# Kernel tuning notes

Measured on AMD Instinct MI355X. Metric: run time of the kernel, lower is better.

Reference implementation:

```python
import jax, jax.numpy as jnp
import numpy as np

B, S, H, D, DM = 2, 512, 8, 32, 256  # batch, seq_len, n_head, d_k, d_model


def setup_inputs() -> dict:
    key = jax.random.key(0)
    ks = jax.random.split(key, 8)
    scale = 0.02
    return {
        "hidden_states": jax.random.normal(ks[0], (B, S, DM), dtype=jnp.float32),
        "rpe": jax.random.normal(ks[1], (B, S, S, D), dtype=jnp.float32),
        "w_q": jax.random.normal(ks[2], (DM, H * D), dtype=jnp.float32) * scale,
        "w_k": jax.random.normal(ks[3], (DM, H * D), dtype=jnp.float32) * scale,
        "w_v": jax.random.normal(ks[4], (DM, H * D), dtype=jnp.float32) * scale,
        "fc_w": jax.random.normal(ks[5], (H * D, DM), dtype=jnp.float32) * scale,
        "fc_b": jnp.zeros((DM,), dtype=jnp.float32),
        "ln_w": jnp.ones((DM,), dtype=jnp.float32),
        "ln_b": jnp.zeros((DM,), dtype=jnp.float32),
        "station_num": 256,
    }


def reference(hidden_states, rpe, w_q, w_k, w_v, fc_w, fc_b, ln_w, ln_b, station_num):
    b, s, dm = hidden_states.shape
    d = rpe.shape[-1]
    h = w_q.shape[1] // d

    def heads(x, w):
        # (b, s, dm) @ (dm, h*d) -> (b, h, s, d)
        return (x @ w).reshape(b, s, h, d).transpose(0, 2, 1, 3)

    q = heads(hidden_states, w_q)
    k = heads(hidden_states, w_k)
    v = heads(hidden_states, w_v)

    # torch: (q.unsqueeze(2) * k.unsqueeze(3) * rpe.unsqueeze(1)).sum(-1)
    # scores[b,h,i,j] = sum_d q[b,h,j,d] * k[b,h,i,d] * rpe[b,i,j,d]
    scores = jnp.einsum('bhjd,bhid,bijd->bhij', q, k, rpe) / jnp.sqrt(jnp.float32(d))

    # shielded mask: column j visible if j < station_num, plus the diagonal
    col = jnp.arange(s) < station_num                  # (s,)
    mask = col[None, :] | jnp.eye(s, dtype=bool)        # (s, s)
    scores = jnp.where(mask[None, None], scores, jnp.float32(-1e10))

    attn = jax.nn.softmax(scores, axis=-1)              # (b, h, s, s)
    out = jnp.einsum('bhij,bhjd->bhid', attn, v)        # (b, h, s, d)
    out = out.transpose(0, 2, 1, 3).reshape(b, s, h * d)

    ctx = out @ fc_w + fc_b + hidden_states             # residual
    mu = jnp.mean(ctx, axis=-1, keepdims=True)
    var = jnp.mean(jnp.square(ctx - mu), axis=-1, keepdims=True)
    ctx = (ctx - mu) / jnp.sqrt(var + 1e-6) * ln_w + ln_b
    return ctx
```

## Files before the change

kernel.cpp:

```cpp
#include <hip/hip_runtime.h>
#include <hip/hip_bf16.h>

#define B_  2
#define S_  512
#define H_  8
#define D_  32
#define DM_ 256
#define HD_ 256
#define NROW 4
#define TI  4

__global__ __launch_bounds__(256) void qkv_kernel(
    const float* __restrict__ hid, const float* __restrict__ wq,
    const float* __restrict__ wk, const float* __restrict__ wv,
    float* __restrict__ qo, float* __restrict__ ko, float* __restrict__ vo)
{
  __shared__ float hs[NROW][DM_];
  const int r0 = blockIdx.x * NROW;
  const float* w   = (blockIdx.y == 0) ? wq : (blockIdx.y == 1) ? wk : wv;
  float*       out = (blockIdx.y == 0) ? qo : (blockIdx.y == 1) ? ko : vo;
  const int tid = threadIdx.x;

  for (int idx = tid; idx < NROW * DM_; idx += 256)
    hs[idx >> 8][idx & 255] = hid[r0 * DM_ + idx];
  __syncthreads();

  float acc[NROW] = {0.f, 0.f, 0.f, 0.f};
  const float* wp = w + tid;
  #pragma unroll 8
  for (int c4 = 0; c4 < DM_ / 4; ++c4) {
    const float w0 = wp[(4 * c4 + 0) * HD_];
    const float w1 = wp[(4 * c4 + 1) * HD_];
    const float w2 = wp[(4 * c4 + 2) * HD_];
    const float w3 = wp[(4 * c4 + 3) * HD_];
    #pragma unroll
    for (int r = 0; r < NROW; ++r) {
      const float4 hv = reinterpret_cast<const float4*>(&hs[r][0])[c4];
      acc[r] = fmaf(hv.x, w0, acc[r]);
      acc[r] = fmaf(hv.y, w1, acc[r]);
      acc[r] = fmaf(hv.z, w2, acc[r]);
      acc[r] = fmaf(hv.w, w3, acc[r]);
    }
  }
  const int h = tid >> 5, d = tid & 31;
  #pragma unroll
  for (int r = 0; r < NROW; ++r) {
    const int g = r0 + r;
    const int b = g >> 9, s = g & (S_ - 1);
    out[((b * H_ + h) * S_ + s) * D_ + d] = acc[r];
  }
}

__device__ __forceinline__ float red8(float x) {
  int i;
  i = __builtin_amdgcn_mov_dpp(__float_as_int(x), 0xB1, 0xf, 0xf, true);
  x += __int_as_float(i);
  i = __builtin_amdgcn_mov_dpp(__float_as_int(x), 0x4E, 0xf, 0xf, true);
  x += __int_as_float(i);
  i = __builtin_amdgcn_mov_dpp(__float_as_int(x), 0x124, 0xf, 0xf, true);
  x += __int_as_float(i);
  return x;
}

__global__ __launch_bounds__(256, 8) void attn_kernel(
    const float* __restrict__ rpe, const float* __restrict__ q_ws,
    const float* __restrict__ k_ws, const float* __restrict__ v_ws,
    const int* __restrict__ station_p, float* __restrict__ o_ws)
{
  __shared__ float p_smem[TI * S_];
  __shared__ float sums[TI];

  const int tid  = threadIdx.x;
  const int w    = tid >> 6, lane = tid & 63;
  const int j8   = lane >> 3, dc = lane & 7;
  const int n    = blockIdx.x;
  const int h    = (n >> 3) & 7;
  const int t    = (n & 7) | ((n >> 6) << 3);
  const int b    = t >> 7;
  const int i0   = (t & 127) * TI;

  int station = station_p[0];
  station = station > S_ ? S_ : (station < 0 ? 0 : station);

  const float* qb = q_ws + (size_t)((b * H_ + h) * S_) * D_;
  const float* kb = k_ws + (size_t)((b * H_ + h) * S_ + i0) * D_;
  const float* vb = v_ws + (size_t)((b * H_ + h) * S_) * D_;
  const float* rb = rpe + ((size_t)b * S_ + i0) * S_ * D_;
  const float sc = 0.17677669529663687f;

  float4 kf[TI];
  #pragma unroll
  for (int ii = 0; ii < TI; ++ii)
    kf[ii] = *reinterpret_cast<const float4*>(kb + ii * D_ + dc * 4);

  for (int jb = w * 8; jb < station; jb += 32) {
    const int j  = jb + j8;
    const int jc = j < S_ ? j : S_ - 1;
    const float4 q4 = *reinterpret_cast<const float4*>(qb + jc * D_ + dc * 4);
    float4 rv[TI];
    #pragma unroll
    for (int ii = 0; ii < TI; ++ii)
      rv[ii] = *reinterpret_cast<const float4*>(
          rb + ii * (S_ * D_) + jc * D_ + dc * 4);
    #pragma unroll
    for (int ii = 0; ii < TI; ++ii) {
      float s = q4.x * kf[ii].x * rv[ii].x;
      s = fmaf(q4.y * kf[ii].y, rv[ii].y, s);
      s = fmaf(q4.z * kf[ii].z, rv[ii].z, s);
      s = fmaf(q4.w * kf[ii].w, rv[ii].w, s);
      s = red8(s);
      if (dc == 0 && j < station) p_smem[ii * S_ + j] = s * sc;
    }
  }
  if (w == 0 && j8 < TI) {
    const int j = i0 + j8;
    if (j >= station) {
      const float4 q4 = *reinterpret_cast<const float4*>(qb + j * D_ + dc * 4);
      const float4 rv = *reinterpret_cast<const float4*>(
          rb + j8 * (S_ * D_) + j * D_ + dc * 4);
      float s = q4.x * kf[j8].x * rv.x;
      s = fmaf(q4.y * kf[j8].y, rv.y, s);
      s = fmaf(q4.z * kf[j8].z, rv.z, s);
      s = fmaf(q4.w * kf[j8].w, rv.w, s);
      s = red8(s);
      if (dc == 0) p_smem[j8 * S_ + j] = s * sc;
    }
  }
  __syncthreads();

  {
    const int r  = w;
    const int ig = i0 + r;
    const bool dx = (ig >= station);
    float m = -1e30f;
    for (int jj = lane; jj < station; jj += 64) m = fmaxf(m, p_smem[r * S_ + jj]);
    const float dv = dx ? p_smem[r * S_ + ig] : -1e30f;
    m = fmaxf(m, dv);
    #pragma unroll
    for (int o = 32; o; o >>= 1) m = fmaxf(m, __shfl_xor(m, o, 64));
    float sum = 0.f;
    for (int jj = lane; jj < station; jj += 64) {
      const float e = __expf(p_smem[r * S_ + jj] - m);
      p_smem[r * S_ + jj] = e;
      sum += e;
    }
    #pragma unroll
    for (int o = 32; o; o >>= 1) sum += __shfl_xor(sum, o, 64);
    if (dx) {
      const float e = __expf(dv - m);
      sum += e;
      if (lane == 0) p_smem[r * S_ + ig] = e;
    }
    if (lane == 0) sums[r] = sum;
  }
  __syncthreads();

  float4 acc[TI];
  #pragma unroll
  for (int ii = 0; ii < TI; ++ii) acc[ii] = make_float4(0.f, 0.f, 0.f, 0.f);

  for (int jb = w * 8; jb < station; jb += 32) {
    const int j  = jb + j8;
    const int jc = j < S_ ? j : S_ - 1;
    const float4 v4 = *reinterpret_cast<const float4*>(vb + jc * D_ + dc * 4);
    #pragma unroll
    for (int ii = 0; ii < TI; ++ii) {
      float pv = 0.f;
      if (j < station) pv = p_smem[ii * S_ + j];
      acc[ii].x = fmaf(pv, v4.x, acc[ii].x);
      acc[ii].y = fmaf(pv, v4.y, acc[ii].y);
      acc[ii].z = fmaf(pv, v4.z, acc[ii].z);
      acc[ii].w = fmaf(pv, v4.w, acc[ii].w);
    }
  }
  if (w == 0 && j8 == 0) {
    #pragma unroll
    for (int ii = 0; ii < TI; ++ii) {
      const int ig = i0 + ii;
      if (ig >= station) {
        const float pv = p_smem[ii * S_ + ig];
        const float4 v4 = *reinterpret_cast<const float4*>(vb + ig * D_ + dc * 4);
        acc[ii].x = fmaf(pv, v4.x, acc[ii].x);
        acc[ii].y = fmaf(pv, v4.y, acc[ii].y);
        acc[ii].z = fmaf(pv, v4.z, acc[ii].z);
        acc[ii].w = fmaf(pv, v4.w, acc[ii].w);
      }
    }
  }
  __syncthreads();

  float4* redv = reinterpret_cast<float4*>(p_smem);
  #pragma unroll
  for (int ii = 0; ii < TI; ++ii) {
    float4 a = acc[ii];
    a.x += __shfl_xor(a.x, 8);
    a.y += __shfl_xor(a.y, 8);
    a.z += __shfl_xor(a.z, 8);
    a.w += __shfl_xor(a.w, 8);
    if ((j8 & 1) == 0)
      redv[((w * 4 + (j8 >> 1)) * TI + ii) * 8 + dc] = a;
  }
  __syncthreads();
  if (tid < TI * 8) {
    const int ii = tid >> 3, d4 = tid & 7;
    float4 a = make_float4(0.f, 0.f, 0.f, 0.f);
    #pragma unroll
    for (int g = 0; g < 16; ++g) {
      const float4 x = redv[(g * TI + ii) * 8 + d4];
      a.x += x.x; a.y += x.y; a.z += x.z; a.w += x.w;
    }
    const float inv = 1.f / sums[ii];
    a.x *= inv; a.y *= inv; a.z *= inv; a.w *= inv;
    reinterpret_cast<float4*>(
        o_ws + (size_t)((b * H_ + h) * S_ + i0 + ii) * D_)[d4] = a;
  }
}

__global__ __launch_bounds__(256) void fc_ln_kernel(
    const float* __restrict__ o_ws, const float* __restrict__ fc_w,
    const float* __restrict__ fc_b, const float* __restrict__ hid,
    const float* __restrict__ ln_w, const float* __restrict__ ln_b,
    float* __restrict__ out)
{
  __shared__ float orow[NROW][HD_];
  __shared__ float red[NROW][4];
  const int tid = threadIdx.x;
  const int r0 = blockIdx.x * NROW;

  for (int idx = tid; idx < NROW * HD_; idx += 256) {
    const int r = idx >> 8, m = idx & 255;
    const int g = r0 + r;
    const int b = g >> 9, i = g & (S_ - 1);
    orow[r][m] = o_ws[((b * H_ + (m >> 5)) * S_ + i) * D_ + (m & 31)];
  }
  __syncthreads();

  float acc[NROW] = {0.f, 0.f, 0.f, 0.f};
  const float* wp = fc_w + tid;
  #pragma unroll 8
  for (int n4 = 0; n4 < HD_ / 4; ++n4) {
    const float w0 = wp[(4 * n4 + 0) * DM_];
    const float w1 = wp[(4 * n4 + 1) * DM_];
    const float w2 = wp[(4 * n4 + 2) * DM_];
    const float w3 = wp[(4 * n4 + 3) * DM_];
    #pragma unroll
    for (int r = 0; r < NROW; ++r) {
      const float4 ov = reinterpret_cast<const float4*>(&orow[r][0])[n4];
      acc[r] = fmaf(ov.x, w0, acc[r]);
      acc[r] = fmaf(ov.y, w1, acc[r]);
      acc[r] = fmaf(ov.z, w2, acc[r]);
      acc[r] = fmaf(ov.w, w3, acc[r]);
    }
  }
  const float bias = fc_b[tid];
  #pragma unroll
  for (int r = 0; r < NROW; ++r) acc[r] += bias + hid[(r0 + r) * DM_ + tid];

  const int w = tid >> 6, lane = tid & 63;
  float mu[NROW];
  #pragma unroll
  for (int r = 0; r < NROW; ++r) {
    float s = acc[r];
    #pragma unroll
    for (int o = 32; o; o >>= 1) s += __shfl_xor(s, o, 64);
    if (lane == 0) red[r][w] = s;
  }
  __syncthreads();
  #pragma unroll
  for (int r = 0; r < NROW; ++r)
    mu[r] = (red[r][0] + red[r][1] + red[r][2] + red[r][3]) * (1.f / DM_);
  __syncthreads();
  #pragma unroll
  for (int r = 0; r < NROW; ++r) {
    const float dd = acc[r] - mu[r];
    float s = dd * dd;
    #pragma unroll
    for (int o = 32; o; o >>= 1) s += __shfl_xor(s, o, 64);
    if (lane == 0) red[r][w] = s;
  }
  __syncthreads();
  const float lw = ln_w[tid], lb = ln_b[tid];
  #pragma unroll
  for (int r = 0; r < NROW; ++r) {
    const float var = (red[r][0] + red[r][1] + red[r][2] + red[r][3]) * (1.f / DM_);
    out[(r0 + r) * DM_ + tid] =
        (acc[r] - mu[r]) * rsqrtf(var + 1e-6f) * lw + lb;
  }
}

extern "C" void kernel_launch(void* const* d_in, const int* in_sizes, int n_in,
                              void* d_out, int out_size, void* d_ws, size_t ws_size,
                              hipStream_t stream) {
  const float* hid = (const float*)d_in[0];
  const float* rpe = (const float*)d_in[1];
  const float* wq  = (const float*)d_in[2];
  const float* wk  = (const float*)d_in[3];
  const float* wv  = (const float*)d_in[4];
  const float* fcw = (const float*)d_in[5];
  const float* fcb = (const float*)d_in[6];
  const float* lnw = (const float*)d_in[7];
  const float* lnb = (const float*)d_in[8];
  const int* station = (const int*)d_in[9];
  float* out = (float*)d_out;

  const size_t per = (size_t)B_ * H_ * S_ * D_;
  float* q_ws = (float*)d_ws;
  float* k_ws = q_ws + per;
  float* v_ws = k_ws + per;
  float* o_ws = v_ws + per;

  dim3 gA(B_ * S_ / NROW, 3);
  qkv_kernel<<<gA, 256, 0, stream>>>(hid, wq, wk, wv, q_ws, k_ws, v_ws);
  attn_kernel<<<B_ * (S_ / TI) * H_, 256, 0, stream>>>(
      rpe, q_ws, k_ws, v_ws, station, o_ws);
  fc_ln_kernel<<<B_ * S_ / NROW, 256, 0, stream>>>(o_ws, fcw, fcb, hid, lnw, lnb, out);
}
```

Measured before the change: 176.9 us.

## Process two heads per attention block to reuse rpe loads across heads

Reorganises the attention tiling so each block handles 2 query rows times 2 heads instead of 4 rows times 1 head, so every rpe tile it loads is used by two heads. This cuts the rpe traffic, which is the dominant memory stream, by about half. Lanes now cover 8 d-elements each, so the cross-lane reduction shrinks to 4 lanes, and the 1/sqrt(d) scale is folded into the Q projection. In exchange the kernel holds more registers (launch bounds drop to 4 blocks per CU) and loads more Q/K/V per block.

```diff
diff --git a/kernel.cpp b/kernel.cpp
--- a/kernel.cpp
+++ b/kernel.cpp
@@ -8,7 +8,9 @@
 #define DM_ 256
 #define HD_ 256
 #define NROW 4
-#define TI  4
+#define TI  2
+#define HC  2
+#define NR  (TI * HC)
 
 __global__ __launch_bounds__(256) void qkv_kernel(
     const float* __restrict__ hid, const float* __restrict__ wq,
@@ -19,6 +21,7 @@
   const int r0 = blockIdx.x * NROW;
   const float* w   = (blockIdx.y == 0) ? wq : (blockIdx.y == 1) ? wk : wv;
   float*       out = (blockIdx.y == 0) ? qo : (blockIdx.y == 1) ? ko : vo;
+  const float mulf = (blockIdx.y == 0) ? 0.17677669529663687f : 1.0f;
   const int tid = threadIdx.x;
 
   for (int idx = tid; idx < NROW * DM_; idx += 256)
@@ -47,90 +50,117 @@
   for (int r = 0; r < NROW; ++r) {
     const int g = r0 + r;
     const int b = g >> 9, s = g & (S_ - 1);
-    out[((b * H_ + h) * S_ + s) * D_ + d] = acc[r];
-  }
-}
-
-__device__ __forceinline__ float red8(float x) {
+    out[((b * H_ + h) * S_ + s) * D_ + d] = acc[r] * mulf;
+  }
+}
+
+__device__ __forceinline__ float red4(float x) {
   int i;
   i = __builtin_amdgcn_mov_dpp(__float_as_int(x), 0xB1, 0xf, 0xf, true);
   x += __int_as_float(i);
   i = __builtin_amdgcn_mov_dpp(__float_as_int(x), 0x4E, 0xf, 0xf, true);
   x += __int_as_float(i);
-  i = __builtin_amdgcn_mov_dpp(__float_as_int(x), 0x124, 0xf, 0xf, true);
-  x += __int_as_float(i);
   return x;
 }
 
-__global__ __launch_bounds__(256, 8) void attn_kernel(
+__global__ __launch_bounds__(256, 4) void attn_kernel(
     const float* __restrict__ rpe, const float* __restrict__ q_ws,
     const float* __restrict__ k_ws, const float* __restrict__ v_ws,
     const int* __restrict__ station_p, float* __restrict__ o_ws)
 {
-  __shared__ float p_smem[TI * S_];
-  __shared__ float sums[TI];
+  __shared__ float p_smem[NR * S_];
+  __shared__ float sums[NR];
 
   const int tid  = threadIdx.x;
   const int w    = tid >> 6, lane = tid & 63;
+  const int j4   = lane >> 2, dq = lane & 3;
   const int j8   = lane >> 3, dc = lane & 7;
   const int n    = blockIdx.x;
-  const int h    = (n >> 3) & 7;
-  const int t    = (n & 7) | ((n >> 6) << 3);
-  const int b    = t >> 7;
-  const int i0   = (t & 127) * TI;
+  const int hg   = (n >> 3) & 3;
+  const int t    = (n & 7) | ((n >> 5) << 3);
+  const int b    = t >> 8;
+  const int i0   = (t & 255) * TI;
+  const int h0   = hg * HC;
+  const int HS   = S_ * D_;
 
   int station = station_p[0];
   station = station > S_ ? S_ : (station < 0 ? 0 : station);
 
-  const float* qb = q_ws + (size_t)((b * H_ + h) * S_) * D_;
-  const float* kb = k_ws + (size_t)((b * H_ + h) * S_ + i0) * D_;
-  const float* vb = v_ws + (size_t)((b * H_ + h) * S_) * D_;
+  const float* qb = q_ws + (size_t)((b * H_ + h0) * S_) * D_;
+  const float* kb = k_ws + (size_t)((b * H_ + h0) * S_ + i0) * D_;
+  const float* vb = v_ws + (size_t)((b * H_ + h0) * S_) * D_;
   const float* rb = rpe + ((size_t)b * S_ + i0) * S_ * D_;
-  const float sc = 0.17677669529663687f;
-
-  float4 kf[TI];
-  #pragma unroll
-  for (int ii = 0; ii < TI; ++ii)
-    kf[ii] = *reinterpret_cast<const float4*>(kb + ii * D_ + dc * 4);
-
-  for (int jb = w * 8; jb < station; jb += 32) {
-    const int j  = jb + j8;
+
+  float4 kf[HC][TI][2];
+  #pragma unroll
+  for (int hh = 0; hh < HC; ++hh)
+    #pragma unroll
+    for (int ii = 0; ii < TI; ++ii) {
+      kf[hh][ii][0] = *reinterpret_cast<const float4*>(kb + hh * HS + ii * D_ + dq * 8);
+      kf[hh][ii][1] = *reinterpret_cast<const float4*>(kb + hh * HS + ii * D_ + dq * 8 + 4);
+    }
+
+  for (int jb = w * 16; jb < station; jb += 64) {
+    const int j  = jb + j4;
     const int jc = j < S_ ? j : S_ - 1;
-    const float4 q4 = *reinterpret_cast<const float4*>(qb + jc * D_ + dc * 4);
-    float4 rv[TI];
-    #pragma unroll
-    for (int ii = 0; ii < TI; ++ii)
-      rv[ii] = *reinterpret_cast<const float4*>(
-          rb + ii * (S_ * D_) + jc * D_ + dc * 4);
+    float4 q[HC][2];
+    #pragma unroll
+    for (int hh = 0; hh < HC; ++hh) {
+      q[hh][0] = *reinterpret_cast<const float4*>(qb + hh * HS + jc * D_ + dq * 8);
+      q[hh][1] = *reinterpret_cast<const float4*>(qb + hh * HS + jc * D_ + dq * 8 + 4);
+    }
+    float4 rv[TI][2];
     #pragma unroll
     for (int ii = 0; ii < TI; ++ii) {
-      float s = q4.x * kf[ii].x * rv[ii].x;
-      s = fmaf(q4.y * kf[ii].y, rv[ii].y, s);
-      s = fmaf(q4.z * kf[ii].z, rv[ii].z, s);
-      s = fmaf(q4.w * kf[ii].w, rv[ii].w, s);
-      s = red8(s);
-      if (dc == 0 && j < station) p_smem[ii * S_ + j] = s * sc;
-    }
-  }
-  if (w == 0 && j8 < TI) {
-    const int j = i0 + j8;
+      rv[ii][0] = *reinterpret_cast<const float4*>(rb + ii * HS + jc * D_ + dq * 8);
+      rv[ii][1] = *reinterpret_cast<const float4*>(rb + ii * HS + jc * D_ + dq * 8 + 4);
+    }
+    #pragma unroll
+    for (int hh = 0; hh < HC; ++hh)
+      #pragma unroll
+      for (int ii = 0; ii < TI; ++ii) {
+        float s = q[hh][0].x * kf[hh][ii][0].x * rv[ii][0].x;
+        s = fmaf(q[hh][0].y * kf[hh][ii][0].y, rv[ii][0].y, s);
+        s = fmaf(q[hh][0].z * kf[hh][ii][0].z, rv[ii][0].z, s);
+        s = fmaf(q[hh][0].w * kf[hh][ii][0].w, rv[ii][0].w, s);
+        s = fmaf(q[hh][1].x * kf[hh][ii][1].x, rv[ii][1].x, s);
+        s = fmaf(q[hh][1].y * kf[hh][ii][1].y, rv[ii][1].y, s);
+        s = fmaf(q[hh][1].z * kf[hh][ii][1].z, rv[ii][1].z, s);
+        s = fmaf(q[hh][1].w * kf[hh][ii][1].w, rv[ii][1].w, s);
+        s = red4(s);
+        if (dq == 0 && j < station) p_smem[(hh * TI + ii) * S_ + j] = s;
+      }
+  }
+  if (w == 0 && j4 < TI) {
+    const int j = i0 + j4;
     if (j >= station) {
-      const float4 q4 = *reinterpret_cast<const float4*>(qb + j * D_ + dc * 4);
-      const float4 rv = *reinterpret_cast<const float4*>(
-          rb + j8 * (S_ * D_) + j * D_ + dc * 4);
-      float s = q4.x * kf[j8].x * rv.x;
-      s = fmaf(q4.y * kf[j8].y, rv.y, s);
-      s = fmaf(q4.z * kf[j8].z, rv.z, s);
-      s = fmaf(q4.w * kf[j8].w, rv.w, s);
-      s = red8(s);
-      if (dc == 0) p_smem[j8 * S_ + j] = s * sc;
+      const float4 r0 = *reinterpret_cast<const float4*>(rb + j4 * HS + j * D_ + dq * 8);
+      const float4 r1 = *reinterpret_cast<const float4*>(rb + j4 * HS + j * D_ + dq * 8 + 4);
+      #pragma unroll
+      for (int hh = 0; hh < HC; ++hh) {
+        const float4 q0 = *reinterpret_cast<const float4*>(qb + hh * HS + j * D_ + dq * 8);
+        const float4 q1 = *reinterpret_cast<const float4*>(qb + hh * HS + j * D_ + dq * 8 + 4);
+        const float4 k0 = *reinterpret_cast<const float4*>(kb + hh * HS + j4 * D_ + dq * 8);
+        const float4 k1 = *reinterpret_cast<const float4*>(kb + hh * HS + j4 * D_ + dq * 8 + 4);
+        float s = q0.x * k0.x * r0.x;
+        s = fmaf(q0.y * k0.y, r0.y, s);
+        s = fmaf(q0.z * k0.z, r0.z, s);
+        s = fmaf(q0.w * k0.w, r0.w, s);
+        s = fmaf(q1.x * k1.x, r1.x, s);
+        s = fmaf(q1.y * k1.y, r1.y, s);
+        s = fmaf(q1.z * k1.z, r1.z, s);
+        s = fmaf(q1.w * k1.w, r1.w, s);
+        s = red4(s);
+        if (dq == 0) p_smem[(hh * TI + j4) * S_ + j] = s;
+      }
     }
   }
   __syncthreads();
 
   {
     const int r  = w;
-    const int ig = i0 + r;
+    const int ii = r & (TI - 1);
+    const int ig = i0 + ii;
     const bool dx = (ig >= station);
     float m = -1e30f;
     for (int jj = lane; jj < station; jj += 64) m = fmaxf(m, p_smem[r * S_ + jj]);
@@ -155,35 +185,45 @@
   }
   __syncthreads();
 
-  float4 acc[TI];
-  #pragma unroll
-  for (int ii = 0; ii < TI; ++ii) acc[ii] = make_float4(0.f, 0.f, 0.f, 0.f);
+  float4 acc[HC][TI];
+  #pragma unroll
+  for (int hh = 0; hh < HC; ++hh)
+    #pragma unroll
+    for (int ii = 0; ii < TI; ++ii) acc[hh][ii] = make_float4(0.f, 0.f, 0.f, 0.f);
 
   for (int jb = w * 8; jb < station; jb += 32) {
     const int j  = jb + j8;
     const int jc = j < S_ ? j : S_ - 1;
-    const float4 v4 = *reinterpret_cast<const float4*>(vb + jc * D_ + dc * 4);
-    #pragma unroll
-    for (int ii = 0; ii < TI; ++ii) {
-      float pv = 0.f;
-      if (j < station) pv = p_smem[ii * S_ + j];
-      acc[ii].x = fmaf(pv, v4.x, acc[ii].x);
-      acc[ii].y = fmaf(pv, v4.y, acc[ii].y);
-      acc[ii].z = fmaf(pv, v4.z, acc[ii].z);
-      acc[ii].w = fmaf(pv, v4.w, acc[ii].w);
-    }
+    float4 v4[HC];
+    #pragma unroll
+    for (int hh = 0; hh < HC; ++hh)
+      v4[hh] = *reinterpret_cast<const float4*>(vb + hh * HS + jc * D_ + dc * 4);
+    #pragma unroll
+    for (int hh = 0; hh < HC; ++hh)
+      #pragma unroll
+      for (int ii = 0; ii < TI; ++ii) {
+        float pv = 0.f;
+        if (j < station) pv = p_smem[(hh * TI + ii) * S_ + j];
+        acc[hh][ii].x = fmaf(pv, v4[hh].x, acc[hh][ii].x);
+        acc[hh][ii].y = fmaf(pv, v4[hh].y, acc[hh][ii].y);
+        acc[hh][ii].z = fmaf(pv, v4[hh].z, acc[hh][ii].z);
+        acc[hh][ii].w = fmaf(pv, v4[hh].w, acc[hh][ii].w);
+      }
   }
   if (w == 0 && j8 == 0) {
     #pragma unroll
     for (int ii = 0; ii < TI; ++ii) {
       const int ig = i0 + ii;
       if (ig >= station) {
-        const float pv = p_smem[ii * S_ + ig];
-        const float4 v4 = *reinterpret_cast<const float4*>(vb + ig * D_ + dc * 4);
-        acc[ii].x = fmaf(pv, v4.x, acc[ii].x);
-        acc[ii].y = fmaf(pv, v4.y, acc[ii].y);
-        acc[ii].z = fmaf(pv, v4.z, acc[ii].z);
-        acc[ii].w = fmaf(pv, v4.w, acc[ii].w);
+        #pragma unroll
+        for (int hh = 0; hh < HC; ++hh) {
+          const float pv = p_smem[(hh * TI + ii) * S_ + ig];
+          const float4 v4 = *reinterpret_cast<const float4*>(vb + hh * HS + ig * D_ + dc * 4);
+          acc[hh][ii].x = fmaf(pv, v4.x, acc[hh][ii].x);
+          acc[hh][ii].y = fmaf(pv, v4.y, acc[hh][ii].y);
+          acc[hh][ii].z = fmaf(pv, v4.z, acc[hh][ii].z);
+          acc[hh][ii].w = fmaf(pv, v4.w, acc[hh][ii].w);
+        }
       }
     }
   }
@@ -191,28 +231,32 @@
 
   float4* redv = reinterpret_cast<float4*>(p_smem);
   #pragma unroll
-  for (int ii = 0; ii < TI; ++ii) {
-    float4 a = acc[ii];
-    a.x += __shfl_xor(a.x, 8);
-    a.y += __shfl_xor(a.y, 8);
-    a.z += __shfl_xor(a.z, 8);
-    a.w += __shfl_xor(a.w, 8);
-    if ((j8 & 1) == 0)
-      redv[((w * 4 + (j8 >> 1)) * TI + ii) * 8 + dc] = a;
-  }
-  __syncthreads();
-  if (tid < TI * 8) {
-    const int ii = tid >> 3, d4 = tid & 7;
+  for (int hh = 0; hh < HC; ++hh)
+    #pragma unroll
+    for (int ii = 0; ii < TI; ++ii) {
+      const int r = hh * TI + ii;
+      float4 a = acc[hh][ii];
+      a.x += __shfl_xor(a.x, 8);
+      a.y += __shfl_xor(a.y, 8);
+      a.z += __shfl_xor(a.z, 8);
+      a.w += __shfl_xor(a.w, 8);
+      if ((j8 & 1) == 0)
+        redv[((w * 4 + (j8 >> 1)) * NR + r) * 8 + dc] = a;
+    }
+  __syncthreads();
+  if (tid < NR * 8) {
+    const int r = tid >> 3, d4 = tid & 7;
     float4 a = make_float4(0.f, 0.f, 0.f, 0.f);
     #pragma unroll
     for (int g = 0; g < 16; ++g) {
-      const float4 x = redv[(g * TI + ii) * 8 + d4];
+      const float4 x = redv[(g * NR + r) * 8 + d4];
       a.x += x.x; a.y += x.y; a.z += x.z; a.w += x.w;
     }
-    const float inv = 1.f / sums[ii];
+    const float inv = 1.f / sums[r];
     a.x *= inv; a.y *= inv; a.z *= inv; a.w *= inv;
+    const int hh = r >> 1, ii = r & 1;
     reinterpret_cast<float4*>(
-        o_ws + (size_t)((b * H_ + h) * S_ + i0 + ii) * D_)[d4] = a;
+        o_ws + (size_t)((b * H_ + h0 + hh) * S_ + i0 + ii) * D_)[d4] = a;
   }
 }
 
@@ -311,7 +355,7 @@
 
   dim3 gA(B_ * S_ / NROW, 3);
   qkv_kernel<<<gA, 256, 0, stream>>>(hid, wq, wk, wv, q_ws, k_ws, v_ws);
-  attn_kernel<<<B_ * (S_ / TI) * H_, 256, 0, stream>>>(
+  attn_kernel<<<B_ * (S_ / TI) * (H_ / HC), 256, 0, stream>>>(
       rpe, q_ws, k_ws, v_ws, station, o_ws);
   fc_ln_kernel<<<B_ * S_ / NROW, 256, 0, stream>>>(o_ws, fcw, fcb, hid, lnw, lnb, out);
 }
```

Result: faster. 156.7 us (-11.4%).
